# Optimization experiments

Hardware: AMD Instinct MI355X
Metric: run time of the kernel (lower is better)

## Reference

```python
import jax, jax.numpy as jnp
import numpy as np

N = 16384      # total nodes (hits)
K = 8          # n_neighbors
NB = 8         # number of graphs in batch
IN_C = 6       # in_channels
HID = 128      # hidden_channels
NCLS = 3       # num_classes
SLOPE = 0.2    # GATv2 leaky_relu negative_slope
BIG = 1e30     # mask value for cross-graph pairs


def setup_inputs() -> dict:
    key = jax.random.key(0)
    ks = jax.random.split(key, 32)
    coord = jax.random.normal(ks[0], (N, 3), dtype=jnp.float32)
    feat = jax.random.normal(ks[1], (N, IN_C), dtype=jnp.float32)
    batch = jnp.sort(jax.random.randint(ks[2], (N,), 0, NB)).astype(jnp.int32)

    def lin_w(k, fan_in, fan_out):
        return (jax.random.normal(k, (fan_in, fan_out), dtype=jnp.float32)
                * np.float32(1.0 / np.sqrt(fan_in)))

    inp = {"coord": coord, "feat": feat, "batch": batch}
    dims = [IN_C, HID, HID]  # input dim of each of the 3 GATv2 layers
    kidx = 3
    for l, din in enumerate(dims):
        inp[f"Wl{l}"] = lin_w(ks[kidx], din, HID); kidx += 1
        inp[f"bl{l}"] = jnp.zeros((HID,), jnp.float32)
        inp[f"Wr{l}"] = lin_w(ks[kidx], din, HID); kidx += 1
        inp[f"br{l}"] = jnp.zeros((HID,), jnp.float32)
        inp[f"att{l}"] = (jax.random.normal(ks[kidx], (HID,), dtype=jnp.float32)
                          * np.float32(1.0 / np.sqrt(HID))); kidx += 1
        inp[f"bias{l}"] = jnp.zeros((HID,), jnp.float32)
    inp["Wf"] = lin_w(ks[kidx], HID, NCLS)
    inp["bf"] = jnp.zeros((NCLS,), jnp.float32)
    return inp


def knn_idx(coord, batch):
    # pairwise squared distances, masked so neighbors stay within the same graph
    d2 = jnp.sum((coord[:, None, :] - coord[None, :, :]) ** 2, axis=-1)  # [N,N]
    d2 = jnp.where(batch[:, None] == batch[None, :], d2, BIG)
    _, idx = jax.lax.top_k(-d2, K)  # [N,K] nearest (includes self at dist 0)
    return idx


def gatv2_layer(x, idx, Wl, bl, Wr, br, att, bias):
    xl = x @ Wl + bl                         # [N,H] source transform
    xr = x @ Wr + br                         # [N,H] target transform
    g = xl[idx]                              # [N,K,H] gather neighbor features
    e = jax.nn.leaky_relu(g + xr[:, None, :], SLOPE)
    logits = e @ att                         # [N,K] attention scores
    alpha = jax.nn.softmax(logits, axis=1)   # softmax over each node's K nbrs
    return jnp.einsum('nk,nkh->nh', alpha, g) + bias


def reference(coord, feat, batch,
              Wl0, bl0, Wr0, br0, att0, bias0,
              Wl1, bl1, Wr1, br1, att1, bias1,
              Wl2, bl2, Wr2, br2, att2, bias2,
              Wf, bf):
    idx = knn_idx(coord, batch)
    x = jax.nn.relu(gatv2_layer(feat, idx, Wl0, bl0, Wr0, br0, att0, bias0))
    x = jax.nn.relu(gatv2_layer(x, idx, Wl1, bl1, Wr1, br1, att1, bias1))
    x = jax.nn.relu(gatv2_layer(x, idx, Wl2, bl2, Wr2, br2, att2, bias2))
    return x @ Wf + bf
```

## Files before the change

kernel.cpp:

```cpp
#include <hip/hip_runtime.h>
#include <hip/hip_bf16.h>
#include <float.h>
#include <limits.h>

#define NNODES 16384
#define KNB 8
#define HIDC 128
#define KNN_CAP 2560

__device__ __forceinline__ unsigned int dpp_shr1_u32(unsigned int v) {
  return (unsigned int)__builtin_amdgcn_update_dpp(0, (int)v, 0x111, 0xF, 0xF, true);
}
__device__ __forceinline__ float wave_sum(float x) {
  x += __int_as_float(__builtin_amdgcn_update_dpp(0, __float_as_int(x), 0xB1, 0xF, 0xF, true));
  x += __int_as_float(__builtin_amdgcn_update_dpp(0, __float_as_int(x), 0x4E, 0xF, 0xF, true));
  x += __int_as_float(__builtin_amdgcn_update_dpp(0, __float_as_int(x), 0x124, 0xF, 0xF, true));
  x += __int_as_float(__builtin_amdgcn_update_dpp(0, __float_as_int(x), 0x128, 0xF, 0xF, true));
  float r0 = __int_as_float(__builtin_amdgcn_readlane(__float_as_int(x), 0));
  float r1 = __int_as_float(__builtin_amdgcn_readlane(__float_as_int(x), 16));
  float r2 = __int_as_float(__builtin_amdgcn_readlane(__float_as_int(x), 32));
  float r3 = __int_as_float(__builtin_amdgcn_readlane(__float_as_int(x), 48));
  return (r0 + r1) + (r2 + r3);
}

__device__ __forceinline__ float dist2(float ax, float ay, float az,
                                       float bx, float by, float bz) {
  float dx = ax - bx, dy = ay - by, dz = az - bz;
  return fmaf(dz, dz, fmaf(dy, dy, dx * dx));
}

__device__ __forceinline__ void insert_survivors(
    unsigned long long m, unsigned int c_lo, unsigned int c_hi,
    unsigned int& llo, unsigned int& lhi, unsigned long long& tau) {
  while (m) {
    int src = __builtin_ctzll(m);
    m &= m - 1;
    unsigned int nlo = (unsigned int)__builtin_amdgcn_readlane((int)c_lo, src);
    unsigned int nhi = (unsigned int)__builtin_amdgcn_readlane((int)c_hi, src);
    unsigned long long nk = ((unsigned long long)nhi << 32) | nlo;
    if (nk >= tau) continue;
    unsigned int plo = dpp_shr1_u32(llo);
    unsigned int phi = dpp_shr1_u32(lhi);
    unsigned long long pk = ((unsigned long long)phi << 32) | plo;
    unsigned long long ck = ((unsigned long long)lhi << 32) | llo;
    if (nk < ck) {
      unsigned long long r = (pk > nk) ? pk : nk;
      llo = (unsigned int)r; lhi = (unsigned int)(r >> 32);
    }
    tau = (((unsigned long long)(unsigned int)__builtin_amdgcn_readlane((int)lhi, 7)) << 32)
          | (unsigned int)__builtin_amdgcn_readlane((int)llo, 7);
  }
}

__global__ void seg_kernel(const int* __restrict__ batch, int* __restrict__ seg) {
  int b = threadIdx.x;
  if (b > 8) return;
  int lo = 0, hi = NNODES;
  while (lo < hi) { int m = (lo + hi) >> 1; if (batch[m] < b) lo = m + 1; else hi = m; }
  seg[b] = lo;
}

__global__ __launch_bounds__(512) void knn_kernel(
    const float* __restrict__ coord, const int* __restrict__ batch,
    const int* __restrict__ seg, int* __restrict__ knn) {
  __shared__ float4 tile[KNN_CAP];
  int t = threadIdx.x;
  int lane = t & 63;
  int n0 = blockIdx.x * 8;
  int n = n0 + (t >> 6);

  int b0 = batch[n0], b7 = batch[n0 + 7], bw = batch[n];
  int smin = seg[b0];
  int emax = seg[b7 + 1];
  int s_w = seg[bw];
  int e_w = seg[bw + 1];
  int win_end = min(emax, smin + KNN_CAP);
  int cnt = win_end - smin;

  for (int i = t; i < cnt; i += 512) {
    const float* cp = coord + (size_t)(smin + i) * 3;
    tile[i] = make_float4(cp[0], cp[1], cp[2], 0.f);
  }

  float cx = coord[n*3+0], cy = coord[n*3+1], cz = coord[n*3+2];

  unsigned long long tau = ~0ull;
  unsigned int llo = 0xFFFFFFFFu, lhi = 0xFFFFFFFFu;

  {
    int j = s_w + (lane & 7);
    bool ok8 = (lane < KNB) && (j < e_w);
    float d = dist2(coord[j*3+0], coord[j*3+1], coord[j*3+2], cx, cy, cz);
    insert_survivors(__ballot(ok8), (unsigned int)j, __float_as_uint(d), llo, lhi, tau);
  }

  __syncthreads();

  int lo_i = s_w - smin;
  int hi_i = min(e_w, win_end) - smin;
  for (int base = lo_i + KNB; base < hi_i; base += 256) {
    unsigned long long k[4];
    #pragma unroll
    for (int q = 0; q < 4; ++q) {
      int i = base + lane + 64 * q;
      bool ok = i < hi_i;
      float4 c = tile[ok ? i : lo_i];
      float d = dist2(c.x, c.y, c.z, cx, cy, cz);
      k[q] = ok ? (((unsigned long long)__float_as_uint(d) << 32) | (unsigned int)(smin + i))
                : ~0ull;
    }
    #pragma unroll
    for (int q = 0; q < 4; ++q) {
      unsigned long long m = __ballot(k[q] < tau);
      if (m) insert_survivors(m, (unsigned int)k[q], (unsigned int)(k[q] >> 32), llo, lhi, tau);
    }
  }

  for (int base = max(s_w + KNB, win_end); base < e_w; base += 64) {
    int j = base + lane;
    bool ok = j < e_w;
    int jc = ok ? j : s_w;
    float d = dist2(coord[jc*3+0], coord[jc*3+1], coord[jc*3+2], cx, cy, cz);
    unsigned long long ckey = ok
        ? (((unsigned long long)__float_as_uint(d) << 32) | (unsigned int)j)
        : ~0ull;
    unsigned long long m = __ballot(ckey < tau);
    if (m) insert_survivors(m, (unsigned int)ckey, (unsigned int)(ckey >> 32), llo, lhi, tau);
  }
  if (lane < KNB) knn[n*KNB + lane] = (int)llo;
}

template<int K>
__global__ __launch_bounds__(256) void lin2_kernel(
    const float* __restrict__ x,
    const float* __restrict__ Wl, const float* __restrict__ bl,
    const float* __restrict__ Wr, const float* __restrict__ br,
    float* __restrict__ xl, float* __restrict__ xr) {
  __shared__ float xs[32 * K];
  int t = threadIdx.x;
  int node0 = blockIdx.x * 32;
  for (int i = t; i < 32 * K; i += 256) xs[i] = x[node0 * K + i];
  __syncthreads();
  int cg = t & 63;
  int ng = t >> 6;
  int c0 = cg * 4;
  bool isR = (c0 >= HIDC);
  const float* W    = isR ? Wr : Wl;
  const float* bias = isR ? br : bl;
  float* dst        = isR ? xr : xl;
  int wc = isR ? (c0 - HIDC) : c0;

  float4 acc[8];
  #pragma unroll
  for (int nn = 0; nn < 8; ++nn) acc[nn] = make_float4(0.f, 0.f, 0.f, 0.f);

  if constexpr (K % 4 == 0) {
    for (int k0 = 0; k0 < K; k0 += 4) {
      float4 xv[8];
      #pragma unroll
      for (int nn = 0; nn < 8; ++nn)
        xv[nn] = *(const float4*)&xs[(ng * 8 + nn) * K + k0];
      #pragma unroll
      for (int q = 0; q < 4; ++q) {
        float4 w = *(const float4*)(W + (size_t)(k0 + q) * HIDC + wc);
        #pragma unroll
        for (int nn = 0; nn < 8; ++nn) {
          float xq = (q == 0) ? xv[nn].x : (q == 1) ? xv[nn].y : (q == 2) ? xv[nn].z : xv[nn].w;
          acc[nn].x = fmaf(xq, w.x, acc[nn].x);
          acc[nn].y = fmaf(xq, w.y, acc[nn].y);
          acc[nn].z = fmaf(xq, w.z, acc[nn].z);
          acc[nn].w = fmaf(xq, w.w, acc[nn].w);
        }
      }
    }
  } else {
    for (int k = 0; k < K; ++k) {
      float4 w = *(const float4*)(W + (size_t)k * HIDC + wc);
      #pragma unroll
      for (int nn = 0; nn < 8; ++nn) {
        float xq = xs[(ng * 8 + nn) * K + k];
        acc[nn].x = fmaf(xq, w.x, acc[nn].x);
        acc[nn].y = fmaf(xq, w.y, acc[nn].y);
        acc[nn].z = fmaf(xq, w.z, acc[nn].z);
        acc[nn].w = fmaf(xq, w.w, acc[nn].w);
      }
    }
  }
  float4 b4 = *(const float4*)(bias + wc);
  #pragma unroll
  for (int nn = 0; nn < 8; ++nn) {
    int node = node0 + ng * 8 + nn;
    float4 o;
    o.x = acc[nn].x + b4.x; o.y = acc[nn].y + b4.y;
    o.z = acc[nn].z + b4.z; o.w = acc[nn].w + b4.w;
    *(float4*)(dst + (size_t)node * HIDC + wc) = o;
  }
}

template<bool FINAL>
__global__ __launch_bounds__(256) void gat_attn_kernel(
    const float* __restrict__ xl, const float* __restrict__ xr,
    const int* __restrict__ knn, const float* __restrict__ att,
    const float* __restrict__ bias, float* __restrict__ xout,
    const float* __restrict__ Wf, const float* __restrict__ bf,
    float* __restrict__ out) {
  int wid = threadIdx.x >> 6;
  int lane = threadIdx.x & 63;
  int n = blockIdx.x * 4 + wid;
  int c0 = 2 * lane, c1 = 2 * lane + 1;
  float2 xr2 = *(const float2*)(xr + (size_t)n * HIDC + c0);
  float2 a2  = *(const float2*)(att + c0);
  int myj = (lane < KNB) ? knn[n * KNB + lane] : 0;
  float g0[8], g1[8], lg[8];
  #pragma unroll
  for (int k = 0; k < 8; ++k) {
    int j = __builtin_amdgcn_readlane(myj, k);
    float2 g = *(const float2*)(xl + (size_t)j * HIDC + c0);
    g0[k] = g.x; g1[k] = g.y;
    float e0 = g.x + xr2.x; e0 = (e0 > 0.f) ? e0 : 0.2f * e0;
    float e1 = g.y + xr2.y; e1 = (e1 > 0.f) ? e1 : 0.2f * e1;
    lg[k] = wave_sum(e0 * a2.x + e1 * a2.y);
  }
  float mx = lg[0];
  #pragma unroll
  for (int k = 1; k < 8; ++k) mx = fmaxf(mx, lg[k]);
  float ssum = 0.f, w[8];
  #pragma unroll
  for (int k = 0; k < 8; ++k) { w[k] = __expf(lg[k] - mx); ssum += w[k]; }
  float inv = 1.f / ssum;
  float o0 = 0.f, o1 = 0.f;
  #pragma unroll
  for (int k = 0; k < 8; ++k) { o0 += w[k] * g0[k]; o1 += w[k] * g1[k]; }
  o0 = fmaxf(fmaf(o0, inv, bias[c0]), 0.f);
  o1 = fmaxf(fmaf(o1, inv, bias[c1]), 0.f);
  if (!FINAL) {
    float2 o; o.x = o0; o.y = o1;
    *(float2*)(xout + (size_t)n * HIDC + c0) = o;
  } else {
    #pragma unroll
    for (int cls = 0; cls < 3; ++cls) {
      float p = wave_sum(o0 * Wf[c0 * 3 + cls] + o1 * Wf[c1 * 3 + cls]);
      if (lane == 0) out[n * 3 + cls] = p + bf[cls];
    }
  }
}

extern "C" void kernel_launch(void* const* d_in, const int* in_sizes, int n_in,
                              void* d_out, int out_size, void* d_ws, size_t ws_size,
                              hipStream_t stream) {
  const float* coord = (const float*)d_in[0];
  const float* feat  = (const float*)d_in[1];
  const int*   batch = (const int*)d_in[2];
  const float* Wl0 = (const float*)d_in[3];
  const float* bl0 = (const float*)d_in[4];
  const float* Wr0 = (const float*)d_in[5];
  const float* br0 = (const float*)d_in[6];
  const float* att0  = (const float*)d_in[7];
  const float* bias0 = (const float*)d_in[8];
  const float* Wl1 = (const float*)d_in[9];
  const float* bl1 = (const float*)d_in[10];
  const float* Wr1 = (const float*)d_in[11];
  const float* br1 = (const float*)d_in[12];
  const float* att1  = (const float*)d_in[13];
  const float* bias1 = (const float*)d_in[14];
  const float* Wl2 = (const float*)d_in[15];
  const float* bl2 = (const float*)d_in[16];
  const float* Wr2 = (const float*)d_in[17];
  const float* br2 = (const float*)d_in[18];
  const float* att2  = (const float*)d_in[19];
  const float* bias2 = (const float*)d_in[20];
  const float* Wf = (const float*)d_in[21];
  const float* bf = (const float*)d_in[22];
  float* out = (float*)d_out;

  char* ws = (char*)d_ws;
  int*   knn = (int*)ws;
  float* xl  = (float*)(ws + (512 << 10));
  float* xr  = xl + (size_t)NNODES * HIDC;
  float* xb0 = xr + (size_t)NNODES * HIDC;
  float* xb1 = xb0 + (size_t)NNODES * HIDC;
  int*   seg = (int*)xb0;

  seg_kernel<<<1, 16, 0, stream>>>(batch, seg);
  knn_kernel<<<NNODES / 8, 512, 0, stream>>>(coord, batch, seg, knn);

  lin2_kernel<6><<<NNODES / 32, 256, 0, stream>>>(feat, Wl0, bl0, Wr0, br0, xl, xr);
  gat_attn_kernel<false><<<NNODES / 4, 256, 0, stream>>>(xl, xr, knn, att0, bias0, xb0,
                                                         nullptr, nullptr, nullptr);

  lin2_kernel<128><<<NNODES / 32, 256, 0, stream>>>(xb0, Wl1, bl1, Wr1, br1, xl, xr);
  gat_attn_kernel<false><<<NNODES / 4, 256, 0, stream>>>(xl, xr, knn, att1, bias1, xb1,
                                                         nullptr, nullptr, nullptr);

  lin2_kernel<128><<<NNODES / 32, 256, 0, stream>>>(xb1, Wl2, bl2, Wr2, br2, xl, xr);
  gat_attn_kernel<true><<<NNODES / 4, 256, 0, stream>>>(xl, xr, knn, att2, bias2, nullptr,
                                                        Wf, bf, out);
}
```

Baseline: 167.0 us.

## Replace ballot-based KNN insertion with per-lane med3 top-8 lists plus threshold rescan

The KNN kernel no longer serializes survivors through a wave-wide sorted list with readlane/DPP shifts. Each lane now keeps its own sorted top-8 distances using fmed3 insertion. A wave-wide 8-round min merge then finds the 8th-smallest distance, and a second pass over the candidates writes the indices whose distance is at or below that threshold. This removes divergent scalar insertion loops but doubles the distance computation. Output order becomes index order rather than distance order, and ties at the threshold are resolved by lowest index.

```diff
diff --git a/kernel.cpp b/kernel.cpp
--- a/kernel.cpp
+++ b/kernel.cpp
@@ -8,9 +8,6 @@
 #define HIDC 128
 #define KNN_CAP 2560
 
-__device__ __forceinline__ unsigned int dpp_shr1_u32(unsigned int v) {
-  return (unsigned int)__builtin_amdgcn_update_dpp(0, (int)v, 0x111, 0xF, 0xF, true);
-}
 __device__ __forceinline__ float wave_sum(float x) {
   x += __int_as_float(__builtin_amdgcn_update_dpp(0, __float_as_int(x), 0xB1, 0xF, 0xF, true));
   x += __int_as_float(__builtin_amdgcn_update_dpp(0, __float_as_int(x), 0x4E, 0xF, 0xF, true));
@@ -23,34 +20,36 @@
   return (r0 + r1) + (r2 + r3);
 }
 
+__device__ __forceinline__ float wave_min_f32(float x) {
+  x = fminf(x, __int_as_float(__builtin_amdgcn_update_dpp(0, __float_as_int(x), 0xB1, 0xF, 0xF, true)));
+  x = fminf(x, __int_as_float(__builtin_amdgcn_update_dpp(0, __float_as_int(x), 0x4E, 0xF, 0xF, true)));
+  x = fminf(x, __int_as_float(__builtin_amdgcn_update_dpp(0, __float_as_int(x), 0x124, 0xF, 0xF, true)));
+  x = fminf(x, __int_as_float(__builtin_amdgcn_update_dpp(0, __float_as_int(x), 0x128, 0xF, 0xF, true)));
+  float r0 = __int_as_float(__builtin_amdgcn_readlane(__float_as_int(x), 0));
+  float r1 = __int_as_float(__builtin_amdgcn_readlane(__float_as_int(x), 16));
+  float r2 = __int_as_float(__builtin_amdgcn_readlane(__float_as_int(x), 32));
+  float r3 = __int_as_float(__builtin_amdgcn_readlane(__float_as_int(x), 48));
+  return fminf(fminf(r0, r1), fminf(r2, r3));
+}
+
 __device__ __forceinline__ float dist2(float ax, float ay, float az,
                                        float bx, float by, float bz) {
   float dx = ax - bx, dy = ay - by, dz = az - bz;
   return fmaf(dz, dz, fmaf(dy, dy, dx * dx));
 }
 
-__device__ __forceinline__ void insert_survivors(
-    unsigned long long m, unsigned int c_lo, unsigned int c_hi,
-    unsigned int& llo, unsigned int& lhi, unsigned long long& tau) {
-  while (m) {
-    int src = __builtin_ctzll(m);
-    m &= m - 1;
-    unsigned int nlo = (unsigned int)__builtin_amdgcn_readlane((int)c_lo, src);
-    unsigned int nhi = (unsigned int)__builtin_amdgcn_readlane((int)c_hi, src);
-    unsigned long long nk = ((unsigned long long)nhi << 32) | nlo;
-    if (nk >= tau) continue;
-    unsigned int plo = dpp_shr1_u32(llo);
-    unsigned int phi = dpp_shr1_u32(lhi);
-    unsigned long long pk = ((unsigned long long)phi << 32) | plo;
-    unsigned long long ck = ((unsigned long long)lhi << 32) | llo;
-    if (nk < ck) {
-      unsigned long long r = (pk > nk) ? pk : nk;
-      llo = (unsigned int)r; lhi = (unsigned int)(r >> 32);
-    }
-    tau = (((unsigned long long)(unsigned int)__builtin_amdgcn_readlane((int)lhi, 7)) << 32)
-          | (unsigned int)__builtin_amdgcn_readlane((int)llo, 7);
-  }
-}
+#define INS8(d)                                   \
+  do {                                            \
+    float _d = (d);                               \
+    l7 = __builtin_amdgcn_fmed3f(_d, l6, l7);     \
+    l6 = __builtin_amdgcn_fmed3f(_d, l5, l6);     \
+    l5 = __builtin_amdgcn_fmed3f(_d, l4, l5);     \
+    l4 = __builtin_amdgcn_fmed3f(_d, l3, l4);     \
+    l3 = __builtin_amdgcn_fmed3f(_d, l2, l3);     \
+    l2 = __builtin_amdgcn_fmed3f(_d, l1, l2);     \
+    l1 = __builtin_amdgcn_fmed3f(_d, l0, l1);     \
+    l0 = fminf(l0, _d);                           \
+  } while (0)
 
 __global__ void seg_kernel(const int* __restrict__ batch, int* __restrict__ seg) {
   int b = threadIdx.x;
@@ -75,59 +74,79 @@
   int s_w = seg[bw];
   int e_w = seg[bw + 1];
   int win_end = min(emax, smin + KNN_CAP);
-  int cnt = win_end - smin;
-
-  for (int i = t; i < cnt; i += 512) {
+  int cnt_fill = win_end - smin;
+
+  for (int i = t; i < cnt_fill; i += 512) {
     const float* cp = coord + (size_t)(smin + i) * 3;
     tile[i] = make_float4(cp[0], cp[1], cp[2], 0.f);
   }
+  __syncthreads();
 
   float cx = coord[n*3+0], cy = coord[n*3+1], cz = coord[n*3+2];
 
-  unsigned long long tau = ~0ull;
-  unsigned int llo = 0xFFFFFFFFu, lhi = 0xFFFFFFFFu;
-
-  {
-    int j = s_w + (lane & 7);
-    bool ok8 = (lane < KNB) && (j < e_w);
-    float d = dist2(coord[j*3+0], coord[j*3+1], coord[j*3+2], cx, cy, cz);
-    insert_survivors(__ballot(ok8), (unsigned int)j, __float_as_uint(d), llo, lhi, tau);
-  }
-
-  __syncthreads();
-
+  float l0 = FLT_MAX, l1 = FLT_MAX, l2 = FLT_MAX, l3 = FLT_MAX,
+        l4 = FLT_MAX, l5 = FLT_MAX, l6 = FLT_MAX, l7 = FLT_MAX;
   int lo_i = s_w - smin;
   int hi_i = min(e_w, win_end) - smin;
-  for (int base = lo_i + KNB; base < hi_i; base += 256) {
-    unsigned long long k[4];
-    #pragma unroll
-    for (int q = 0; q < 4; ++q) {
-      int i = base + lane + 64 * q;
-      bool ok = i < hi_i;
-      float4 c = tile[ok ? i : lo_i];
-      float d = dist2(c.x, c.y, c.z, cx, cy, cz);
-      k[q] = ok ? (((unsigned long long)__float_as_uint(d) << 32) | (unsigned int)(smin + i))
-                : ~0ull;
-    }
-    #pragma unroll
-    for (int q = 0; q < 4; ++q) {
-      unsigned long long m = __ballot(k[q] < tau);
-      if (m) insert_survivors(m, (unsigned int)k[q], (unsigned int)(k[q] >> 32), llo, lhi, tau);
-    }
-  }
-
-  for (int base = max(s_w + KNB, win_end); base < e_w; base += 64) {
+  #pragma unroll 2
+  for (int base = lo_i; base < hi_i; base += 64) {
+    int i = base + lane;
+    bool ok = i < hi_i;
+    float4 c = tile[ok ? i : lo_i];
+    float d = dist2(c.x, c.y, c.z, cx, cy, cz);
+    d = ok ? d : FLT_MAX;
+    INS8(d);
+  }
+  for (int base = max(s_w, win_end); base < e_w; base += 64) {
     int j = base + lane;
     bool ok = j < e_w;
     int jc = ok ? j : s_w;
     float d = dist2(coord[jc*3+0], coord[jc*3+1], coord[jc*3+2], cx, cy, cz);
-    unsigned long long ckey = ok
-        ? (((unsigned long long)__float_as_uint(d) << 32) | (unsigned int)j)
-        : ~0ull;
-    unsigned long long m = __ballot(ckey < tau);
-    if (m) insert_survivors(m, (unsigned int)ckey, (unsigned int)(ckey >> 32), llo, lhi, tau);
-  }
-  if (lane < KNB) knn[n*KNB + lane] = (int)llo;
+    d = ok ? d : FLT_MAX;
+    INS8(d);
+  }
+
+  float T = 0.f;
+  #pragma unroll
+  for (int r = 0; r < KNB; ++r) {
+    float m = wave_min_f32(l0);
+    T = m;
+    unsigned long long msk = __ballot(l0 == m);
+    int p = (int)__builtin_ctzll(msk);
+    if (lane == p) {
+      l0 = l1; l1 = l2; l2 = l3; l3 = l4; l4 = l5; l5 = l6; l6 = l7; l7 = FLT_MAX;
+    }
+  }
+
+  int cnt = 0;
+  for (int base = lo_i; base < hi_i; base += 64) {
+    int i = base + lane;
+    bool ok = i < hi_i;
+    float4 c = tile[ok ? i : lo_i];
+    float d = dist2(c.x, c.y, c.z, cx, cy, cz);
+    bool win = ok && (d <= T);
+    unsigned long long msk = __ballot(win);
+    if (msk) {
+      int rank = __popcll(msk & ((1ull << lane) - 1ull));
+      int slot = cnt + rank;
+      if (win && slot < KNB) knn[n*KNB + slot] = smin + i;
+      cnt += __popcll(msk);
+    }
+  }
+  for (int base = max(s_w, win_end); base < e_w; base += 64) {
+    int j = base + lane;
+    bool ok = j < e_w;
+    int jc = ok ? j : s_w;
+    float d = dist2(coord[jc*3+0], coord[jc*3+1], coord[jc*3+2], cx, cy, cz);
+    bool win = ok && (d <= T);
+    unsigned long long msk = __ballot(win);
+    if (msk) {
+      int rank = __popcll(msk & ((1ull << lane) - 1ull));
+      int slot = cnt + rank;
+      if (win && slot < KNB) knn[n*KNB + slot] = j;
+      cnt += __popcll(msk);
+    }
+  }
 }
 
 template<int K>
```

Result: faster. 152.7 us (-8.6%).
